# Kernel optimization log

Measured on AMD Instinct MI355X. Metric: run time of the kernel, lower is better.

The kernel has to match this reference:

```python
import jax, jax.numpy as jnp
import numpy as np

N = 50000          # nodes
E = 800000         # random edges (self-loops appended inside reference)
IN = 32            # input feature dim
HID = 128          # hidden dim (heads * per-head channels)
HEADS = 4
CH = HID // HEADS  # 32 per-head channels
OUT = 6
SLOPE = 0.2        # GATv2 leaky_relu negative slope (PyG default)
EPS = 1e-5


def setup_inputs() -> dict:
    key = jax.random.key(0)
    ks = jax.random.split(key, 24)
    def rn(k, shape, scale=0.05):
        return jax.random.normal(k, shape, dtype=jnp.float32) * scale
    return {
        "x": jax.random.normal(ks[0], (N, IN), dtype=jnp.float32),
        "edge_index": jax.random.randint(ks[1], (2, E), 0, N, dtype=jnp.int32),
        # GATv2 layer 1 (separate source/target transforms, share_weights=False)
        "Wl1": rn(ks[2], (IN, HID)), "Wr1": rn(ks[3], (IN, HID)),
        "att1": rn(ks[4], (HEADS, CH)), "bias1": jnp.zeros((HID,), jnp.float32),
        "g1": jnp.ones((HID,), jnp.float32), "b1": jnp.zeros((HID,), jnp.float32),
        # GATv2 layer 2
        "Wl2": rn(ks[5], (HID, HID)), "Wr2": rn(ks[6], (HID, HID)),
        "att2": rn(ks[7], (HEADS, CH)), "bias2": jnp.zeros((HID,), jnp.float32),
        "g2": jnp.ones((HID,), jnp.float32), "b2": jnp.zeros((HID,), jnp.float32),
        # prediction head: Linear(HID, HID//2) -> ReLU -> Linear(HID//2, OUT)
        "Wp1": rn(ks[8], (HID, HID // 2)), "bp1": jnp.zeros((HID // 2,), jnp.float32),
        "Wp2": rn(ks[9], (HID // 2, OUT)), "bp2": jnp.zeros((OUT,), jnp.float32),
        # uncertainty head: Linear(HID, HID//4) -> ReLU -> Linear(HID//4, OUT) -> Softplus
        "Wu1": rn(ks[10], (HID, HID // 4)), "bu1": jnp.zeros((HID // 4,), jnp.float32),
        "Wu2": rn(ks[11], (HID // 4, OUT)), "bu2": jnp.zeros((OUT,), jnp.float32),
    }


def _gatv2(x, src, dst, Wl, Wr, att, bias):
    # GATv2: e_ij = att . leaky_relu(Wl x_j + Wr x_i); softmax over incoming edges of i
    n = x.shape[0]
    xl = (x @ Wl).reshape(n, HEADS, CH)   # source (message) transform
    xr = (x @ Wr).reshape(n, HEADS, CH)   # target transform
    el = xl[src]                           # [E, H, C] gather
    e = jax.nn.leaky_relu(el + xr[dst], SLOPE)
    s = jnp.einsum('ehc,hc->eh', e, att)   # [E, H] attention logits
    m = jax.ops.segment_max(s, dst, num_segments=n)          # stable softmax per dst
    a = jnp.exp(s - m[dst])
    denom = jax.ops.segment_sum(a, dst, num_segments=n)
    alpha = a / denom[dst]                 # [E, H]
    out = jax.ops.segment_sum(el * alpha[:, :, None], dst, num_segments=n)
    return out.reshape(n, HID) + bias


def _ln(h, g, b):
    mu = jnp.mean(h, axis=-1, keepdims=True)
    v = jnp.var(h, axis=-1, keepdims=True)
    return (h - mu) * jax.lax.rsqrt(v + EPS) * g + b


def reference(x, edge_index, Wl1, Wr1, att1, bias1, g1, b1,
              Wl2, Wr2, att2, bias2, g2, b2,
              Wp1, bp1, Wp2, bp2, Wu1, bu1, Wu2, bu2):
    n = x.shape[0]
    loops = jnp.arange(n, dtype=edge_index.dtype)
    ei = jnp.concatenate([edge_index, jnp.stack([loops, loops])], axis=1)
    src, dst = ei[0], ei[1]
    h = _gatv2(x, src, dst, Wl1, Wr1, att1, bias1)
    h = jax.nn.elu(_ln(h, g1, b1))
    h2 = _gatv2(h, src, dst, Wl2, Wr2, att2, bias2)
    h2 = _ln(h2, g2, b2)
    h = jax.nn.elu(h + h2)
    pred = jnp.maximum(h @ Wp1 + bp1, 0.0) @ Wp2 + bp2
    uncertainty = jax.nn.softplus(jnp.maximum(h @ Wu1 + bu1, 0.0) @ Wu2 + bu2)
    return pred, uncertainty
```

## Files before the change

kernel.cpp:

```cpp
#include <hip/hip_runtime.h>
#include <hip/hip_bf16.h>
#include <math.h>

#define HID 128
#define HEADS 4
#define CH 32
#define OUTD 6
#define SLOPE 0.2f
#define LNEPS 1e-5f

static inline int cdiv(int a, int b) { return (a + b - 1) / b; }

__device__ __forceinline__ unsigned short f2bf(float f) {
    unsigned int u = __builtin_bit_cast(unsigned int, f);
    u += 0x7FFFu + ((u >> 16) & 1u);
    return (unsigned short)(u >> 16);
}
__device__ __forceinline__ float bflo(unsigned int u) {
    return __builtin_bit_cast(float, u << 16);
}
__device__ __forceinline__ float bfhi(unsigned int u) {
    return __builtin_bit_cast(float, u & 0xFFFF0000u);
}


__global__ void k_count_rank(const int* __restrict__ ei, int E, int n,
                             int* __restrict__ deg, int* __restrict__ epos) {
    int e = blockIdx.x * 256 + threadIdx.x;
    int EA = E + n;
    if (e >= EA) return;
    int dst = (e < E) ? ei[E + e] : (e - E);
    epos[e] = atomicAdd(&deg[dst], 1);
}

__global__ __launch_bounds__(1024) void k_scan1(const int* __restrict__ deg, int n,
                                                int* __restrict__ ex, int* __restrict__ bsum) {
    __shared__ int sw[16];
    int i = blockIdx.x * 1024 + threadIdx.x;
    int v = (i < n) ? deg[i] : 0;
    int lane = threadIdx.x & 63, w = threadIdx.x >> 6;
    int x = v;
    #pragma unroll
    for (int d = 1; d < 64; d <<= 1) {
        int t = __shfl_up(x, d);
        if (lane >= d) x += t;
    }
    if (lane == 63) sw[w] = x;
    __syncthreads();
    if (w == 0) {
        int t = (lane < 16) ? sw[lane] : 0;
        #pragma unroll
        for (int d = 1; d < 16; d <<= 1) {
            int u = __shfl_up(t, d);
            if (lane >= d) t += u;
        }
        if (lane < 16) sw[lane] = t;
    }
    __syncthreads();
    int woff = (w > 0) ? sw[w - 1] : 0;
    int incl = x + woff;
    if (i < n) ex[i] = incl - v;
    if (threadIdx.x == 1023) bsum[blockIdx.x] = incl;
}

__global__ void k_scan2(int* __restrict__ bsum, int nb) {
    int lane = threadIdx.x;
    int v = (lane < nb) ? bsum[lane] : 0;
    int x = v;
    #pragma unroll
    for (int d = 1; d < 64; d <<= 1) {
        int t = __shfl_up(x, d);
        if (lane >= d) x += t;
    }
    if (lane < nb) bsum[lane] = x - v;
}

__global__ __launch_bounds__(1024) void k_scan3(int* __restrict__ ex, const int* __restrict__ bsum, int n) {
    int i = blockIdx.x * 1024 + threadIdx.x;
    if (i < n) ex[i] += bsum[blockIdx.x];
}

__global__ void k_scatter(const int* __restrict__ ei, const int* __restrict__ epos,
                          const int* __restrict__ offsets, int E, int n,
                          int* __restrict__ csr_src) {
    int e = blockIdx.x * 256 + threadIdx.x;
    int EA = E + n;
    if (e >= EA) return;
    int src, dst;
    if (e < E) { src = ei[e]; dst = ei[E + e]; }
    else       { src = dst = e - E; }
    csr_src[offsets[dst] + epos[e]] = src;
}

template <int K>
__global__ __launch_bounds__(256) void dual_linear(const float* __restrict__ X,
                                                   const float* __restrict__ Wl,
                                                   const float* __restrict__ Wr,
                                                   unsigned short* __restrict__ outL,
                                                   unsigned short* __restrict__ outR, int n) {
    __shared__ float sX[64][K + 4];
    int tid = threadIdx.x;
    int tx = tid & 63;
    int ty = tid >> 6;
    int node0 = blockIdx.x * 64;

    constexpr int C4 = K / 4;
    constexpr int NQ = (64 * C4) / 256;
    #pragma unroll
    for (int q = 0; q < NQ; ++q) {
        int g = q * 256 + tid;
        int row = g / C4, c4 = g % C4;
        int gn = node0 + row;
        float4 v = make_float4(0.f, 0.f, 0.f, 0.f);
        if (gn < n) v = *(const float4*)&X[(size_t)gn * K + c4 * 4];
        *(float4*)&sX[row][c4 * 4] = v;
    }
    __syncthreads();

    const float* Wbase = (tx < 32) ? (Wl + tx * 4) : (Wr + (tx - 32) * 4);

    float4 acc[16];
    #pragma unroll
    for (int i = 0; i < 16; ++i) acc[i] = make_float4(0.f, 0.f, 0.f, 0.f);

    #pragma unroll 2
    for (int k4 = 0; k4 < K / 4; ++k4) {
        const float* wp = Wbase + (size_t)k4 * 4 * HID;
        float4 w0 = *(const float4*)(wp);
        float4 w1 = *(const float4*)(wp + HID);
        float4 w2 = *(const float4*)(wp + 2 * HID);
        float4 w3 = *(const float4*)(wp + 3 * HID);
        #pragma unroll
        for (int i = 0; i < 16; ++i) {
            float4 xq = *(const float4*)&sX[ty * 16 + i][k4 * 4];
            acc[i].x = fmaf(xq.x, w0.x, acc[i].x);
            acc[i].y = fmaf(xq.x, w0.y, acc[i].y);
            acc[i].z = fmaf(xq.x, w0.z, acc[i].z);
            acc[i].w = fmaf(xq.x, w0.w, acc[i].w);
            acc[i].x = fmaf(xq.y, w1.x, acc[i].x);
            acc[i].y = fmaf(xq.y, w1.y, acc[i].y);
            acc[i].z = fmaf(xq.y, w1.z, acc[i].z);
            acc[i].w = fmaf(xq.y, w1.w, acc[i].w);
            acc[i].x = fmaf(xq.z, w2.x, acc[i].x);
            acc[i].y = fmaf(xq.z, w2.y, acc[i].y);
            acc[i].z = fmaf(xq.z, w2.z, acc[i].z);
            acc[i].w = fmaf(xq.z, w2.w, acc[i].w);
            acc[i].x = fmaf(xq.w, w3.x, acc[i].x);
            acc[i].y = fmaf(xq.w, w3.y, acc[i].y);
            acc[i].z = fmaf(xq.w, w3.z, acc[i].z);
            acc[i].w = fmaf(xq.w, w3.w, acc[i].w);
        }
    }

    int c = tx * 4;
    unsigned short* basep = (c < HID) ? outL : outR;
    int cc = (c < HID) ? c : c - HID;
    #pragma unroll
    for (int i = 0; i < 16; ++i) {
        int gn = node0 + ty * 16 + i;
        if (gn < n) {
            ushort4 o;
            o.x = f2bf(acc[i].x); o.y = f2bf(acc[i].y);
            o.z = f2bf(acc[i].z); o.w = f2bf(acc[i].w);
            *(ushort4*)&basep[(size_t)gn * HID + cc] = o;
        }
    }
}


struct GatAcc {
    float den;
    float nb[8];
};

template <bool CHECKED>
__device__ __forceinline__ void gat_edge(uint4 r, bool valid,
                                         const float4& xrA, const float4& xrB,
                                         const float4& atA, const float4& atB,
                                         GatAcc& g) {
    float e0 = bflo(r.x), e1 = bfhi(r.x);
    float e2 = bflo(r.y), e3 = bfhi(r.y);
    float e4 = bflo(r.z), e5 = bfhi(r.z);
    float e6 = bflo(r.w), e7 = bfhi(r.w);
    float v0 = e0 + xrA.x; v0 = fmaxf(v0, SLOPE * v0);
    float v1 = e1 + xrA.y; v1 = fmaxf(v1, SLOPE * v1);
    float v2 = e2 + xrA.z; v2 = fmaxf(v2, SLOPE * v2);
    float v3 = e3 + xrA.w; v3 = fmaxf(v3, SLOPE * v3);
    float v4 = e4 + xrB.x; v4 = fmaxf(v4, SLOPE * v4);
    float v5 = e5 + xrB.y; v5 = fmaxf(v5, SLOPE * v5);
    float v6 = e6 + xrB.z; v6 = fmaxf(v6, SLOPE * v6);
    float v7 = e7 + xrB.w; v7 = fmaxf(v7, SLOPE * v7);
    float t = v0 * atA.x;
    t = fmaf(v1, atA.y, t);
    t = fmaf(v2, atA.z, t);
    t = fmaf(v3, atA.w, t);
    t = fmaf(v4, atB.x, t);
    t = fmaf(v5, atB.y, t);
    t = fmaf(v6, atB.z, t);
    t = fmaf(v7, atB.w, t);
    t += __shfl_xor(t, 1);
    t += __shfl_xor(t, 2);
    float a = __expf(t);
    if (CHECKED) a = valid ? a : 0.f;
    g.den += a;
    g.nb[0] = fmaf(a, e0, g.nb[0]);
    g.nb[1] = fmaf(a, e1, g.nb[1]);
    g.nb[2] = fmaf(a, e2, g.nb[2]);
    g.nb[3] = fmaf(a, e3, g.nb[3]);
    g.nb[4] = fmaf(a, e4, g.nb[4]);
    g.nb[5] = fmaf(a, e5, g.nb[5]);
    g.nb[6] = fmaf(a, e6, g.nb[6]);
    g.nb[7] = fmaf(a, e7, g.nb[7]);
}

__global__ __launch_bounds__(256) void gat_aggr(const unsigned short* __restrict__ xl,
                                                const unsigned short* __restrict__ xr,
                                                const int* __restrict__ csr_src,
                                                const int* __restrict__ offsets,
                                                const int* __restrict__ deg,
                                                const float* __restrict__ att,
                                                const float* __restrict__ bias,
                                                const float* __restrict__ gamma,
                                                const float* __restrict__ beta,
                                                const float* __restrict__ hprev,
                                                float* __restrict__ hout,
                                                int n, int layer) {
    int wave = threadIdx.x >> 6;
    int lane = threadIdx.x & 63;
    int dst = blockIdx.x * 4 + wave;
    if (dst >= n) return;

    int lc = lane & 15;
    int eg = lane >> 4;
    int c0 = lc * 8;
    unsigned cb = (unsigned)(lc * 16);

    float4 atA = *(const float4*)&att[c0];
    float4 atB = *(const float4*)&att[c0 + 4];
    const char* xlb = (const char*)xl;

    uint4 xrr = *(const uint4*)((const char*)xr + (unsigned)dst * 256u + cb);
    float4 xrA = make_float4(bflo(xrr.x), bfhi(xrr.x), bflo(xrr.y), bfhi(xrr.y));
    float4 xrB = make_float4(bflo(xrr.z), bfhi(xrr.z), bflo(xrr.w), bfhi(xrr.w));

    int start = offsets[dst];
    int cnt = deg[dst];
    const int* sp = csr_src + start;

    GatAcc g;
    g.den = 0.f;
    #pragma unroll
    for (int j = 0; j < 8; ++j) g.nb[j] = 0.f;

    for (int base = 0; base < cnt; base += 64) {
        int rem = cnt - base;
        int lim = rem < 64 ? rem : 64;
        int vidx = (lane < lim) ? sp[base + lane] : 0;
        int fq = lim >> 2;
        int q = 0;
        for (; q + 2 <= fq; q += 2) {
            int slot0 = q * 4 + eg;
            int s0 = __shfl(vidx, slot0);
            int s1 = __shfl(vidx, slot0 + 4);
            uint4 r0 = *(const uint4*)(xlb + (((unsigned)s0 << 8) + cb));
            uint4 r1 = *(const uint4*)(xlb + (((unsigned)s1 << 8) + cb));
            gat_edge<false>(r0, true, xrA, xrB, atA, atB, g);
            gat_edge<false>(r1, true, xrA, xrB, atA, atB, g);
        }
        if (q < fq) {
            int slot0 = q * 4 + eg;
            int s0 = __shfl(vidx, slot0);
            uint4 r0 = *(const uint4*)(xlb + (((unsigned)s0 << 8) + cb));
            gat_edge<false>(r0, true, xrA, xrB, atA, atB, g);
        }
        int tail = lim & 3;
        if (tail) {
            int slot0 = fq * 4 + eg;
            int s0 = __shfl(vidx, slot0);
            uint4 r0 = *(const uint4*)(xlb + (((unsigned)s0 << 8) + cb));
            gat_edge<true>(r0, eg < tail, xrA, xrB, atA, atB, g);
        }
    }

    g.den += __shfl_xor(g.den, 16);
    g.den += __shfl_xor(g.den, 32);
    #pragma unroll
    for (int j = 0; j < 8; ++j) {
        g.nb[j] += __shfl_xor(g.nb[j], 16);
        g.nb[j] += __shfl_xor(g.nb[j], 32);
    }

    float inv = 1.f / g.den;
    float4 bA = *(const float4*)&bias[c0];
    float4 bB = *(const float4*)&bias[c0 + 4];
    float v[8];
    v[0] = fmaf(g.nb[0], inv, bA.x);
    v[1] = fmaf(g.nb[1], inv, bA.y);
    v[2] = fmaf(g.nb[2], inv, bA.z);
    v[3] = fmaf(g.nb[3], inv, bA.w);
    v[4] = fmaf(g.nb[4], inv, bB.x);
    v[5] = fmaf(g.nb[5], inv, bB.y);
    v[6] = fmaf(g.nb[6], inv, bB.z);
    v[7] = fmaf(g.nb[7], inv, bB.w);

    float s1 = 0.f, s2 = 0.f;
    #pragma unroll
    for (int j = 0; j < 8; ++j) {
        s1 += v[j];
        s2 = fmaf(v[j], v[j], s2);
    }
    #pragma unroll
    for (int d = 1; d < 16; d <<= 1) {
        s1 += __shfl_xor(s1, d);
        s2 += __shfl_xor(s2, d);
    }
    float mu = s1 * (1.f / 128.f);
    float var = s2 * (1.f / 128.f) - mu * mu;
    float rs = rsqrtf(var + LNEPS);

    float4 gA = *(const float4*)&gamma[c0];
    float4 gB = *(const float4*)&gamma[c0 + 4];
    float4 beA = *(const float4*)&beta[c0];
    float4 beB = *(const float4*)&beta[c0 + 4];
    float y[8];
    y[0] = (v[0] - mu) * rs * gA.x + beA.x;
    y[1] = (v[1] - mu) * rs * gA.y + beA.y;
    y[2] = (v[2] - mu) * rs * gA.z + beA.z;
    y[3] = (v[3] - mu) * rs * gA.w + beA.w;
    y[4] = (v[4] - mu) * rs * gB.x + beB.x;
    y[5] = (v[5] - mu) * rs * gB.y + beB.y;
    y[6] = (v[6] - mu) * rs * gB.z + beB.z;
    y[7] = (v[7] - mu) * rs * gB.w + beB.w;

    if (layer == 2) {
        const float* hp = &hprev[(size_t)dst * HID + c0];
        float4 hA = *(const float4*)hp;
        float4 hB = *(const float4*)(hp + 4);
        y[0] += hA.x; y[1] += hA.y; y[2] += hA.z; y[3] += hA.w;
        y[4] += hB.x; y[5] += hB.y; y[6] += hB.z; y[7] += hB.w;
    }
    #pragma unroll
    for (int j = 0; j < 8; ++j)
        y[j] = (y[j] > 0.f) ? y[j] : (__expf(y[j]) - 1.f);

    if (eg == 0) {
        float* op = &hout[(size_t)dst * HID + c0];
        *(float4*)op = make_float4(y[0], y[1], y[2], y[3]);
        *(float4*)(op + 4) = make_float4(y[4], y[5], y[6], y[7]);
    }
}

__global__ __launch_bounds__(256) void k_heads(const float* __restrict__ hf,
                                               const float* __restrict__ Wp1, const float* __restrict__ bp1,
                                               const float* __restrict__ Wp2, const float* __restrict__ bp2,
                                               const float* __restrict__ Wu1, const float* __restrict__ bu1,
                                               const float* __restrict__ Wu2, const float* __restrict__ bu2,
                                               float* __restrict__ out, int n) {
    __shared__ float sXH[64 * 132];
    __shared__ float sW[32 * 96];
    __shared__ float sW2[64 * 6 + 32 * 6];
    int tid = threadIdx.x;
    int node0 = blockIdx.x * 64;

    for (int i = tid; i < 576; i += 256) sW2[i] = (i < 384) ? Wp2[i] : Wu2[i - 384];

    {
        int row = tid >> 2, seg = tid & 3;
        int gn = node0 + row;
        const float* src = &hf[(size_t)gn * HID + seg * 32];
        float* dst = &sXH[row * 132 + seg * 32];
        #pragma unroll
        for (int q = 0; q < 8; ++q) {
            float4 v = make_float4(0.f, 0.f, 0.f, 0.f);
            if (gn < n) v = *(const float4*)&src[q * 4];
            *(float4*)&dst[q * 4] = v;
        }
    }

    int cg = tid & 15;
    int ng = tid >> 4;
    int c0 = cg * 6;

    float acc[4][6];
    #pragma unroll
    for (int i = 0; i < 4; ++i)
        #pragma unroll
        for (int j = 0; j < 6; ++j) acc[i][j] = 0.f;

    for (int kc = 0; kc < HID; kc += 32) {
        __syncthreads();
        #pragma unroll
        for (int q = 0; q < 3; ++q) {
            int g = q * 256 + tid;
            int r = g / 24, c4 = g % 24;
            int c = c4 * 4;
            const float* src = (c < 64) ? &Wp1[(size_t)(kc + r) * 64 + c]
                                        : &Wu1[(size_t)(kc + r) * 32 + (c - 64)];
            *(float4*)&sW[r * 96 + c] = *(const float4*)src;
        }
        __syncthreads();
        #pragma unroll
        for (int k = 0; k < 32; ++k) {
            const float* wr = &sW[k * 96 + c0];
            float w0 = wr[0], w1 = wr[1], w2 = wr[2], w3 = wr[3], w4 = wr[4], w5 = wr[5];
            #pragma unroll
            for (int i = 0; i < 4; ++i) {
                float xv = sXH[(ng * 4 + i) * 132 + kc + k];
                acc[i][0] = fmaf(xv, w0, acc[i][0]);
                acc[i][1] = fmaf(xv, w1, acc[i][1]);
                acc[i][2] = fmaf(xv, w2, acc[i][2]);
                acc[i][3] = fmaf(xv, w3, acc[i][3]);
                acc[i][4] = fmaf(xv, w4, acc[i][4]);
                acc[i][5] = fmaf(xv, w5, acc[i][5]);
            }
        }
    }

    __syncthreads();
    float bv[6];
    #pragma unroll
    for (int j = 0; j < 6; ++j) {
        int c = c0 + j;
        bv[j] = (c < 64) ? bp1[c] : bu1[c - 64];
    }
    #pragma unroll
    for (int i = 0; i < 4; ++i) {
        int row = ng * 4 + i;
        #pragma unroll
        for (int j = 0; j < 6; ++j) {
            float v = acc[i][j] + bv[j];
            sXH[row * 97 + c0 + j] = fmaxf(v, 0.f);
        }
    }
    __syncthreads();

    int nl = tid & 63;
    int g = tid >> 6;
    int node = node0 + nl;
    float a0 = 0.f, a1 = 0.f, a2 = 0.f;
    if (g < 2) {
        int j0 = 3 * g;
        const float* hrow = &sXH[nl * 97];
        #pragma unroll 8
        for (int k = 0; k < 64; ++k) {
            float hv = hrow[k];
            a0 = fmaf(hv, sW2[k * 6 + j0], a0);
            a1 = fmaf(hv, sW2[k * 6 + j0 + 1], a1);
            a2 = fmaf(hv, sW2[k * 6 + j0 + 2], a2);
        }
        if (node < n) {
            size_t pb = (size_t)node * 6 + j0;
            out[pb]     = a0 + bp2[j0];
            out[pb + 1] = a1 + bp2[j0 + 1];
            out[pb + 2] = a2 + bp2[j0 + 2];
        }
    } else {
        int j0 = 3 * (g - 2);
        const float* hrow = &sXH[nl * 97 + 64];
        #pragma unroll 8
        for (int k = 0; k < 32; ++k) {
            float hv = hrow[k];
            a0 = fmaf(hv, sW2[384 + k * 6 + j0], a0);
            a1 = fmaf(hv, sW2[384 + k * 6 + j0 + 1], a1);
            a2 = fmaf(hv, sW2[384 + k * 6 + j0 + 2], a2);
        }
        if (node < n) {
            float z0 = a0 + bu2[j0], z1 = a1 + bu2[j0 + 1], z2 = a2 + bu2[j0 + 2];
            size_t ub = (size_t)n * 6 + (size_t)node * 6 + j0;
            out[ub]     = fmaxf(z0, 0.f) + log1pf(__expf(-fabsf(z0)));
            out[ub + 1] = fmaxf(z1, 0.f) + log1pf(__expf(-fabsf(z1)));
            out[ub + 2] = fmaxf(z2, 0.f) + log1pf(__expf(-fabsf(z2)));
        }
    }
}


extern "C" void kernel_launch(void* const* d_in, const int* in_sizes, int n_in,
                              void* d_out, int out_size, void* d_ws, size_t ws_size,
                              hipStream_t stream) {
    const float* x   = (const float*)d_in[0];
    const int*   ei  = (const int*)d_in[1];
    const float* Wl1 = (const float*)d_in[2];
    const float* Wr1 = (const float*)d_in[3];
    const float* att1 = (const float*)d_in[4];
    const float* bias1 = (const float*)d_in[5];
    const float* g1 = (const float*)d_in[6];
    const float* b1 = (const float*)d_in[7];
    const float* Wl2 = (const float*)d_in[8];
    const float* Wr2 = (const float*)d_in[9];
    const float* att2 = (const float*)d_in[10];
    const float* bias2 = (const float*)d_in[11];
    const float* g2 = (const float*)d_in[12];
    const float* b2 = (const float*)d_in[13];
    const float* Wp1 = (const float*)d_in[14];
    const float* bp1 = (const float*)d_in[15];
    const float* Wp2 = (const float*)d_in[16];
    const float* bp2 = (const float*)d_in[17];
    const float* Wu1 = (const float*)d_in[18];
    const float* bu1 = (const float*)d_in[19];
    const float* Wu2 = (const float*)d_in[20];
    const float* bu2 = (const float*)d_in[21];

    int N_ = in_sizes[0] / 32;
    int E_ = in_sizes[1] / 2;
    int EA = E_ + N_;

    char* p = (char*)d_ws;
    size_t fbytes = (size_t)N_ * HID * sizeof(float);
    unsigned short* xl = (unsigned short*)p; p += fbytes / 2;
    unsigned short* xr = (unsigned short*)p; p += fbytes / 2;
    float* h  = (float*)p; p += fbytes;
    float* hf = (float*)p; p += fbytes;
    auto align16 = [](size_t s) { return (s + 15) & ~(size_t)15; };
    int* deg     = (int*)p; p += align16((size_t)N_ * 4);
    int* offsets = (int*)p; p += align16((size_t)N_ * 4);
    int* bsum    = (int*)p; p += 64 * 4;
    int* csr_src = (int*)p; p += align16((size_t)EA * 4);
    int* epos = (int*)hf;

    hipMemsetAsync(deg, 0, (size_t)N_ * 4, stream);

    int nScan = cdiv(N_, 1024);
    k_count_rank<<<cdiv(EA, 256), 256, 0, stream>>>(ei, E_, N_, deg, epos);
    k_scan1<<<nScan, 1024, 0, stream>>>(deg, N_, offsets, bsum);
    k_scan2<<<1, 64, 0, stream>>>(bsum, nScan);
    k_scan3<<<nScan, 1024, 0, stream>>>(offsets, bsum, N_);
    k_scatter<<<cdiv(EA, 256), 256, 0, stream>>>(ei, epos, offsets, E_, N_, csr_src);

    dual_linear<32><<<cdiv(N_, 64), 256, 0, stream>>>(x, Wl1, Wr1, xl, xr, N_);
    gat_aggr<<<cdiv(N_, 4), 256, 0, stream>>>(xl, xr, csr_src, offsets, deg,
                                              att1, bias1, g1, b1, nullptr, h, N_, 1);
    dual_linear<128><<<cdiv(N_, 64), 256, 0, stream>>>(h, Wl2, Wr2, xl, xr, N_);
    gat_aggr<<<cdiv(N_, 4), 256, 0, stream>>>(xl, xr, csr_src, offsets, deg,
                                              att2, bias2, g2, b2, h, hf, N_, 2);
    k_heads<<<cdiv(N_, 64), 256, 0, stream>>>(hf, Wp1, bp1, Wp2, bp2,
                                              Wu1, bu1, Wu2, bu2, (float*)d_out, N_);
}
```

Baseline: 366.1 us.

## Place self-loops at segment start, halve linear tiles, unroll GAT gather by four

Self-loop edges are no longer counted by atomics. Degrees start at 1, each self-loop is written at its segment's first CSR slot during the scan fix-up, and random edges take the ranks after it. The dual_linear blocks shrink to 128 threads over 32 nodes, which doubles the grid for better occupancy on 50k nodes. The GAT aggregation loop now issues four independent gathers per iteration instead of two, hoisting the channel offset, to raise memory-level parallelism at some register cost.

New measurement: 380.6 us. 4.0% more time.

```diff
diff --git a/kernel.cpp b/kernel.cpp
--- a/kernel.cpp
+++ b/kernel.cpp
@@ -24,12 +24,16 @@
 }
 
 
-__global__ void k_count_rank(const int* __restrict__ ei, int E, int n,
+__global__ void k_init_deg(int* __restrict__ deg, int n) {
+    int i = blockIdx.x * 256 + threadIdx.x;
+    if (i < n) deg[i] = 1;
+}
+
+__global__ void k_count_rank(const int* __restrict__ ei, int E,
                              int* __restrict__ deg, int* __restrict__ epos) {
     int e = blockIdx.x * 256 + threadIdx.x;
-    int EA = E + n;
-    if (e >= EA) return;
-    int dst = (e < E) ? ei[E + e] : (e - E);
+    if (e >= E) return;
+    int dst = ei[E + e];
     epos[e] = atomicAdd(&deg[dst], 1);
 }
 
@@ -75,40 +79,42 @@
     if (lane < nb) bsum[lane] = x - v;
 }
 
-__global__ __launch_bounds__(1024) void k_scan3(int* __restrict__ ex, const int* __restrict__ bsum, int n) {
+__global__ __launch_bounds__(1024) void k_scan3(int* __restrict__ ex, const int* __restrict__ bsum,
+                                                int n, int* __restrict__ csr_src) {
     int i = blockIdx.x * 1024 + threadIdx.x;
-    if (i < n) ex[i] += bsum[blockIdx.x];
+    if (i < n) {
+        int off = ex[i] + bsum[blockIdx.x];
+        ex[i] = off;
+        csr_src[off] = i;
+    }
 }
 
 __global__ void k_scatter(const int* __restrict__ ei, const int* __restrict__ epos,
-                          const int* __restrict__ offsets, int E, int n,
+                          const int* __restrict__ offsets, int E,
                           int* __restrict__ csr_src) {
     int e = blockIdx.x * 256 + threadIdx.x;
-    int EA = E + n;
-    if (e >= EA) return;
-    int src, dst;
-    if (e < E) { src = ei[e]; dst = ei[E + e]; }
-    else       { src = dst = e - E; }
+    if (e >= E) return;
+    int src = ei[e], dst = ei[E + e];
     csr_src[offsets[dst] + epos[e]] = src;
 }
 
 template <int K>
-__global__ __launch_bounds__(256) void dual_linear(const float* __restrict__ X,
+__global__ __launch_bounds__(128) void dual_linear(const float* __restrict__ X,
                                                    const float* __restrict__ Wl,
                                                    const float* __restrict__ Wr,
                                                    unsigned short* __restrict__ outL,
                                                    unsigned short* __restrict__ outR, int n) {
-    __shared__ float sX[64][K + 4];
+    __shared__ float sX[32][K + 4];
     int tid = threadIdx.x;
     int tx = tid & 63;
     int ty = tid >> 6;
-    int node0 = blockIdx.x * 64;
+    int node0 = blockIdx.x * 32;
 
     constexpr int C4 = K / 4;
-    constexpr int NQ = (64 * C4) / 256;
+    constexpr int NQ = (32 * C4) / 128;
     #pragma unroll
     for (int q = 0; q < NQ; ++q) {
-        int g = q * 256 + tid;
+        int g = q * 128 + tid;
         int row = g / C4, c4 = g % C4;
         int gn = node0 + row;
         float4 v = make_float4(0.f, 0.f, 0.f, 0.f);
@@ -237,7 +243,7 @@
 
     float4 atA = *(const float4*)&att[c0];
     float4 atB = *(const float4*)&att[c0 + 4];
-    const char* xlb = (const char*)xl;
+    const char* xlcb = (const char*)xl + cb;
 
     uint4 xrr = *(const uint4*)((const char*)xr + (unsigned)dst * 256u + cb);
     float4 xrA = make_float4(bflo(xrr.x), bfhi(xrr.x), bflo(xrr.y), bfhi(xrr.y));
@@ -258,26 +264,32 @@
         int vidx = (lane < lim) ? sp[base + lane] : 0;
         int fq = lim >> 2;
         int q = 0;
-        for (; q + 2 <= fq; q += 2) {
-            int slot0 = q * 4 + eg;
-            int s0 = __shfl(vidx, slot0);
-            int s1 = __shfl(vidx, slot0 + 4);
-            uint4 r0 = *(const uint4*)(xlb + (((unsigned)s0 << 8) + cb));
-            uint4 r1 = *(const uint4*)(xlb + (((unsigned)s1 << 8) + cb));
+        for (; q + 4 <= fq; q += 4) {
+            int slot = q * 4 + eg;
+            int s0 = __shfl(vidx, slot);
+            int s1 = __shfl(vidx, slot + 4);
+            int s2 = __shfl(vidx, slot + 8);
+            int s3 = __shfl(vidx, slot + 12);
+            uint4 r0 = *(const uint4*)(xlcb + ((unsigned)s0 << 8));
+            uint4 r1 = *(const uint4*)(xlcb + ((unsigned)s1 << 8));
+            uint4 r2 = *(const uint4*)(xlcb + ((unsigned)s2 << 8));
+            uint4 r3 = *(const uint4*)(xlcb + ((unsigned)s3 << 8));
             gat_edge<false>(r0, true, xrA, xrB, atA, atB, g);
             gat_edge<false>(r1, true, xrA, xrB, atA, atB, g);
-        }
-        if (q < fq) {
-            int slot0 = q * 4 + eg;
-            int s0 = __shfl(vidx, slot0);
-            uint4 r0 = *(const uint4*)(xlb + (((unsigned)s0 << 8) + cb));
+            gat_edge<false>(r2, true, xrA, xrB, atA, atB, g);
+            gat_edge<false>(r3, true, xrA, xrB, atA, atB, g);
+        }
+        for (; q < fq; ++q) {
+            int slot = q * 4 + eg;
+            int s0 = __shfl(vidx, slot);
+            uint4 r0 = *(const uint4*)(xlcb + ((unsigned)s0 << 8));
             gat_edge<false>(r0, true, xrA, xrB, atA, atB, g);
         }
         int tail = lim & 3;
         if (tail) {
-            int slot0 = fq * 4 + eg;
-            int s0 = __shfl(vidx, slot0);
-            uint4 r0 = *(const uint4*)(xlb + (((unsigned)s0 << 8) + cb));
+            int slot = fq * 4 + eg;
+            int s0 = __shfl(vidx, slot);
+            uint4 r0 = *(const uint4*)(xlcb + ((unsigned)s0 << 8));
             gat_edge<true>(r0, eg < tail, xrA, xrB, atA, atB, g);
         }
     }
@@ -518,19 +530,18 @@
     int* csr_src = (int*)p; p += align16((size_t)EA * 4);
     int* epos = (int*)hf;
 
-    hipMemsetAsync(deg, 0, (size_t)N_ * 4, stream);
-
     int nScan = cdiv(N_, 1024);
-    k_count_rank<<<cdiv(EA, 256), 256, 0, stream>>>(ei, E_, N_, deg, epos);
+    k_init_deg<<<cdiv(N_, 256), 256, 0, stream>>>(deg, N_);
+    k_count_rank<<<cdiv(E_, 256), 256, 0, stream>>>(ei, E_, deg, epos);
     k_scan1<<<nScan, 1024, 0, stream>>>(deg, N_, offsets, bsum);
     k_scan2<<<1, 64, 0, stream>>>(bsum, nScan);
-    k_scan3<<<nScan, 1024, 0, stream>>>(offsets, bsum, N_);
-    k_scatter<<<cdiv(EA, 256), 256, 0, stream>>>(ei, epos, offsets, E_, N_, csr_src);
-
-    dual_linear<32><<<cdiv(N_, 64), 256, 0, stream>>>(x, Wl1, Wr1, xl, xr, N_);
+    k_scan3<<<nScan, 1024, 0, stream>>>(offsets, bsum, N_, csr_src);
+    k_scatter<<<cdiv(E_, 256), 256, 0, stream>>>(ei, epos, offsets, E_, csr_src);
+
+    dual_linear<32><<<cdiv(N_, 32), 128, 0, stream>>>(x, Wl1, Wr1, xl, xr, N_);
     gat_aggr<<<cdiv(N_, 4), 256, 0, stream>>>(xl, xr, csr_src, offsets, deg,
                                               att1, bias1, g1, b1, nullptr, h, N_, 1);
-    dual_linear<128><<<cdiv(N_, 64), 256, 0, stream>>>(h, Wl2, Wr2, xl, xr, N_);
+    dual_linear<128><<<cdiv(N_, 32), 128, 0, stream>>>(h, Wl2, Wr2, xl, xr, N_);
     gat_aggr<<<cdiv(N_, 4), 256, 0, stream>>>(xl, xr, csr_src, offsets, deg,
                                               att2, bias2, g2, b2, h, hf, N_, 2);
     k_heads<<<cdiv(N_, 64), 256, 0, stream>>>(hf, Wp1, bp1, Wp2, bp2,
```
